# Kernel tuning notes

Hardware: AMD Instinct MI355X
Metric: run time of the kernel (lower is better)

Reference implementation:

```python
import jax, jax.numpy as jnp
import numpy as np

SEQ, HID = 4096, 1024
NEG_INF = -10000000000.0


def setup_inputs() -> dict:
    key = jax.random.key(0)
    ks = jax.random.split(key, 6)
    s = 1.0 / np.sqrt(HID)
    return {
        "query": jax.random.normal(ks[0], (SEQ, HID), jnp.float32),
        "key": jax.random.normal(ks[1], (SEQ, HID), jnp.float32),
        "value": jax.random.normal(ks[2], (SEQ, HID), jnp.float32),
        # SASRec causal mask: allowed positions are 1, masked are 0
        "mask": jnp.tril(jnp.ones((SEQ, SEQ), jnp.int32)),
        "Wq": jax.random.normal(ks[3], (HID, HID), jnp.float32) * s,
        "Wk": jax.random.normal(ks[4], (HID, HID), jnp.float32) * s,
        "Wv": jax.random.normal(ks[5], (HID, HID), jnp.float32) * s,
    }


def reference(query, key, value, mask, Wq, Wk, Wv):
    # nn.Linear(bias=False): y = x @ W.T
    Q = query @ Wq.T   # [S, H]
    K = key @ Wk.T     # [S, H]
    V = value @ Wv.T   # [S, H]
    scale = jnp.sqrt(jnp.asarray(HID, Q.dtype))
    energy = (Q @ K.T) / scale                      # [S, S]
    energy = jnp.where(mask == 0, NEG_INF, energy)  # masked_fill
    attention = jax.nn.softmax(energy, axis=-1)     # [S, S]
    x = attention @ V                               # dropout is identity in eval
    return (x, attention)
```

## Files before the change

kernel.cpp:

```cpp
#include <hip/hip_runtime.h>

#define SEQ 4096
#define HID 1024

typedef _Float16 f16x4 __attribute__((ext_vector_type(4)));
typedef _Float16 f16x8 __attribute__((ext_vector_type(8)));
typedef float    f32x4 __attribute__((ext_vector_type(4)));

__device__ __forceinline__ void gld16(const void* g, void* l) {
    __builtin_amdgcn_global_load_lds(
        (const __attribute__((address_space(1))) unsigned int*)g,
        (__attribute__((address_space(3))) unsigned int*)l, 16, 0, 0);
}

__global__ __launch_bounds__(256) void cast3_f32_f16(
    const float4* __restrict__ a, const float4* __restrict__ b,
    const float4* __restrict__ c,
    f16x4* __restrict__ da, f16x4* __restrict__ db, f16x4* __restrict__ dc,
    int n4) {
    int t = blockIdx.x * 256 + threadIdx.x;
    if (t >= n4) return;
    float4 va = a[t], vb = b[t], vc = c[t];
    f16x4 oa = {(_Float16)va.x, (_Float16)va.y, (_Float16)va.z, (_Float16)va.w};
    f16x4 ob = {(_Float16)vb.x, (_Float16)vb.y, (_Float16)vb.z, (_Float16)vb.w};
    f16x4 oc = {(_Float16)vc.x, (_Float16)vc.y, (_Float16)vc.z, (_Float16)vc.w};
    da[t] = oa; db[t] = ob; dc[t] = oc;
}

__global__ __launch_bounds__(256) void transpose_f16(
    const _Float16* __restrict__ src, _Float16* __restrict__ dst,
    int R, int C) {
    __shared__ _Float16 tile[32][33];
    int c0 = blockIdx.x * 32, r0 = blockIdx.y * 32;
    int tr = threadIdx.x >> 5, tc = threadIdx.x & 31;
#pragma unroll
    for (int q = 0; q < 4; ++q)
        tile[tr + q * 8][tc] = src[(size_t)(r0 + tr + q * 8) * C + c0 + tc];
    __syncthreads();
#pragma unroll
    for (int q = 0; q < 4; ++q)
        dst[(size_t)(c0 + tr + q * 8) * R + r0 + tc] = tile[tc][tr + q * 8];
}

template <typename OutT, bool TRI_SKIP, bool TRI_K, int ZMODE>
__global__ __launch_bounds__(256) void gemm_nt(
    const _Float16* __restrict__ A, const _Float16* __restrict__ Bt,
    OutT* __restrict__ C, int M, int N, int K, float scale,
    long sA, long sB, long sC, int KC) {
    __shared__ __attribute__((aligned(16))) _Float16 As[128 * 32];
    __shared__ __attribute__((aligned(16))) _Float16 Bs[128 * 32];

    const int bm = blockIdx.y, bn = blockIdx.x;
    if (TRI_SKIP && bn > bm) return;
    if (ZMODE == 1) {
        A  += (long)blockIdx.z * sA;
        Bt += (long)blockIdx.z * sB;
        C  += (long)blockIdx.z * sC;
    }
    int kend = TRI_K ? min(K, (bm + 1) * 128) : K;
    int kstart = 0;
    if (ZMODE == 2) {
        kstart = blockIdx.z * KC;
        if (kstart >= kend) return;
        kend = min(kend, kstart + KC);
    }

    const int tid = threadIdx.x;
    const int tr  = tid >> 2;
    const int tc8 = (tid & 3) * 8;

    const _Float16* Ab = A  + (size_t)bm * 128 * K;
    const _Float16* Bb = Bt + (size_t)bn * 128 * K;

    const int wave = tid >> 6;
    const int lane = tid & 63;
    const int wm = (wave >> 1) * 64;
    const int wn = (wave & 1) * 64;
    const int lr = lane & 15;
    const int lk = (lane >> 4) * 8;

    f32x4 acc[4][4];
#pragma unroll
    for (int i = 0; i < 4; ++i)
#pragma unroll
        for (int j = 0; j < 4; ++j) acc[i][j] = (f32x4)0.0f;

    for (int k0 = kstart; k0 < kend; k0 += 32) {
        gld16(Ab + (size_t)tr * K        + k0 + tc8, &As[tr * 32 + tc8]);
        gld16(Ab + (size_t)(64 + tr) * K + k0 + tc8, &As[(64 + tr) * 32 + tc8]);
        gld16(Bb + (size_t)tr * K        + k0 + tc8, &Bs[tr * 32 + tc8]);
        gld16(Bb + (size_t)(64 + tr) * K + k0 + tc8, &Bs[(64 + tr) * 32 + tc8]);
        __syncthreads();

        f16x8 af[4], bfr[4];
#pragma unroll
        for (int i = 0; i < 4; ++i)
            af[i] = *(const f16x8*)&As[(wm + i * 16 + lr) * 32 + lk];
#pragma unroll
        for (int j = 0; j < 4; ++j)
            bfr[j] = *(const f16x8*)&Bs[(wn + j * 16 + lr) * 32 + lk];
#pragma unroll
        for (int i = 0; i < 4; ++i)
#pragma unroll
            for (int j = 0; j < 4; ++j)
                acc[i][j] = __builtin_amdgcn_mfma_f32_16x16x32_f16(
                    af[i], bfr[j], acc[i][j], 0, 0, 0);
        __syncthreads();
    }

    const int er = (lane >> 4) * 4;
    const int ec = lane & 15;
#pragma unroll
    for (int i = 0; i < 4; ++i) {
#pragma unroll
        for (int j = 0; j < 4; ++j) {
            const int row0 = bm * 128 + wm + i * 16 + er;
            const int col  = bn * 128 + wn + j * 16 + ec;
#pragma unroll
            for (int r = 0; r < 4; ++r) {
                const size_t idx = (size_t)(row0 + r) * N + col;
                const float val = acc[i][j][r] * scale;
                if (ZMODE == 2)
                    atomicAdd((float*)&C[idx], val);
                else
                    C[idx] = (OutT)val;
            }
        }
    }
}

__global__ __launch_bounds__(256) void softmax_causal(
    float* __restrict__ E, _Float16* __restrict__ P, int S) {
    __shared__ float rowbuf[SEQ];
    __shared__ float red[8];
    const int i   = blockIdx.x;
    const int tid = threadIdx.x;
    const int wv  = tid >> 6, ln = tid & 63;
    float* Erow = E + (size_t)i * S;

    float lmax = -INFINITY;
    for (int j = tid; j <= i; j += 256) {
        float v = Erow[j];
        rowbuf[j] = v;
        lmax = fmaxf(lmax, v);
    }
#pragma unroll
    for (int o = 32; o > 0; o >>= 1) lmax = fmaxf(lmax, __shfl_down(lmax, o, 64));
    if (ln == 0) red[wv] = lmax;
    __syncthreads();
    if (tid == 0)
        red[4] = fmaxf(fmaxf(red[0], red[1]), fmaxf(red[2], red[3]));
    __syncthreads();
    const float rmax = red[4];

    float lsum = 0.0f;
    for (int j = tid; j <= i; j += 256) {
        float e = __expf(rowbuf[j] - rmax);
        rowbuf[j] = e;
        lsum += e;
    }
#pragma unroll
    for (int o = 32; o > 0; o >>= 1) lsum += __shfl_down(lsum, o, 64);
    __syncthreads();
    if (ln == 0) red[wv] = lsum;
    __syncthreads();
    if (tid == 0)
        red[4] = red[0] + red[1] + red[2] + red[3];
    __syncthreads();
    const float rinv = 1.0f / red[4];

    _Float16* Prow = P + (size_t)i * S;
    for (int j = tid; j < S; j += 256) {
        float a = (j <= i) ? rowbuf[j] * rinv : 0.0f;
        Erow[j] = a;
        Prow[j] = (_Float16)a;
    }
}

extern "C" void kernel_launch(void* const* d_in, const int* in_sizes, int n_in,
                              void* d_out, int out_size, void* d_ws, size_t ws_size,
                              hipStream_t stream) {
    const float* q  = (const float*)d_in[0];
    const float* k  = (const float*)d_in[1];
    const float* v  = (const float*)d_in[2];
    const float* Wq = (const float*)d_in[4];
    const float* Wk = (const float*)d_in[5];
    const float* Wv = (const float*)d_in[6];

    float* out_x   = (float*)d_out;
    float* out_att = out_x + (size_t)SEQ * HID;

    char* ws = (char*)d_ws;
    const size_t SH = (size_t)SEQ * HID * sizeof(_Float16);
    const size_t HH = (size_t)HID * HID * sizeof(_Float16);
    _Float16* qh  = (_Float16*)(ws);
    _Float16* kh  = (_Float16*)(ws + SH);
    _Float16* vh  = (_Float16*)(ws + 2 * SH);
    _Float16* wqh = (_Float16*)(ws + 3 * SH);
    _Float16* wkh = (_Float16*)(ws + 3 * SH + HH);
    _Float16* wvh = (_Float16*)(ws + 3 * SH + 2 * HH);
    _Float16* Qh  = (_Float16*)(ws + 3 * SH + 3 * HH);
    _Float16* Kh  = (_Float16*)(ws + 4 * SH + 3 * HH);
    _Float16* Vh  = (_Float16*)(ws + 5 * SH + 3 * HH);
    _Float16* VT  = (_Float16*)(ws + 6 * SH + 3 * HH);
    _Float16* Ph  = (_Float16*)(ws + 7 * SH + 3 * HH);

    hipMemsetAsync(out_x, 0, (size_t)SEQ * HID * sizeof(float), stream);

    cast3_f32_f16<<<SEQ * HID / 4 / 256, 256, 0, stream>>>(
        (const float4*)q, (const float4*)k, (const float4*)v,
        (f16x4*)qh, (f16x4*)kh, (f16x4*)vh, SEQ * HID / 4);
    cast3_f32_f16<<<HID * HID / 4 / 256, 256, 0, stream>>>(
        (const float4*)Wq, (const float4*)Wk, (const float4*)Wv,
        (f16x4*)wqh, (f16x4*)wkh, (f16x4*)wvh, HID * HID / 4);

    gemm_nt<_Float16, false, false, 1><<<dim3(HID / 128, SEQ / 128, 3), 256, 0, stream>>>(
        qh, wqh, Qh, SEQ, HID, HID, 1.0f,
        (long)SEQ * HID, (long)HID * HID, (long)SEQ * HID, 0);

    transpose_f16<<<dim3(HID / 32, SEQ / 32), 256, 0, stream>>>(Vh, VT, SEQ, HID);

    gemm_nt<float, true, false, 0><<<dim3(SEQ / 128, SEQ / 128), 256, 0, stream>>>(
        Qh, Kh, out_att, SEQ, SEQ, HID, 0.03125f, 0, 0, 0, 0);

    softmax_causal<<<SEQ, 256, 0, stream>>>(out_att, Ph, SEQ);

    gemm_nt<float, false, true, 2><<<dim3(HID / 128, SEQ / 128, 4), 256, 0, stream>>>(
        Ph, VT, out_x, SEQ, HID, SEQ, 1.0f, 0, 0, 0, 1024);
}
```

Before: 331.8 us.

## Store energy in fp16 scratch, merge casts, direct-store single-chunk PV, finer split-K

The QK^T GEMM now writes fp16 energies to a workspace buffer instead of fp32 into the attention output. Softmax reads that buffer, writes fp32 attention once, and overwrites the fp16 buffer in place with probabilities only up to the causal block limit. This drops the fp32 read and the extra write of the full output. The two cast kernels are merged into one launch. The PV split-K is doubled to 8 chunks of 512, and chunks that cover the whole causal range store directly instead of using atomics. Rounding energies to fp16 before softmax adds precision risk, and storing directly on top of the memset is only correct because the output is zeroed first.

```diff
diff --git a/kernel.cpp b/kernel.cpp
--- a/kernel.cpp
+++ b/kernel.cpp
@@ -13,18 +13,27 @@
         (__attribute__((address_space(3))) unsigned int*)l, 16, 0, 0);
 }
 
-__global__ __launch_bounds__(256) void cast3_f32_f16(
-    const float4* __restrict__ a, const float4* __restrict__ b,
-    const float4* __restrict__ c,
-    f16x4* __restrict__ da, f16x4* __restrict__ db, f16x4* __restrict__ dc,
-    int n4) {
+__global__ __launch_bounds__(256) void cast_all(
+    const float4* __restrict__ q, const float4* __restrict__ k,
+    const float4* __restrict__ v,
+    const float4* __restrict__ wq, const float4* __restrict__ wk,
+    const float4* __restrict__ wv,
+    f16x4* __restrict__ qh, f16x4* __restrict__ kh, f16x4* __restrict__ vh,
+    f16x4* __restrict__ wqh, f16x4* __restrict__ wkh, f16x4* __restrict__ wvh,
+    int nX4, int nW4) {
     int t = blockIdx.x * 256 + threadIdx.x;
-    if (t >= n4) return;
-    float4 va = a[t], vb = b[t], vc = c[t];
+    const float4 *a, *b, *c; f16x4 *da, *db, *dc; int idx;
+    if (t < nX4) { a = q; b = k; c = v; da = qh; db = kh; dc = vh; idx = t; }
+    else {
+        idx = t - nX4;
+        if (idx >= nW4) return;
+        a = wq; b = wk; c = wv; da = wqh; db = wkh; dc = wvh;
+    }
+    float4 va = a[idx], vb = b[idx], vc = c[idx];
     f16x4 oa = {(_Float16)va.x, (_Float16)va.y, (_Float16)va.z, (_Float16)va.w};
     f16x4 ob = {(_Float16)vb.x, (_Float16)vb.y, (_Float16)vb.z, (_Float16)vb.w};
     f16x4 oc = {(_Float16)vc.x, (_Float16)vc.y, (_Float16)vc.z, (_Float16)vc.w};
-    da[t] = oa; db[t] = ob; dc[t] = oc;
+    da[idx] = oa; db[idx] = ob; dc[idx] = oc;
 }
 
 __global__ __launch_bounds__(256) void transpose_f16(
@@ -59,9 +68,11 @@
     }
     int kend = TRI_K ? min(K, (bm + 1) * 128) : K;
     int kstart = 0;
+    bool single = false;
     if (ZMODE == 2) {
         kstart = blockIdx.z * KC;
         if (kstart >= kend) return;
+        single = (kend <= KC);
         kend = min(kend, kstart + KC);
     }
 
@@ -120,7 +131,7 @@
             for (int r = 0; r < 4; ++r) {
                 const size_t idx = (size_t)(row0 + r) * N + col;
                 const float val = acc[i][j][r] * scale;
-                if (ZMODE == 2)
+                if (ZMODE == 2 && !single)
                     atomicAdd((float*)&C[idx], val);
                 else
                     C[idx] = (OutT)val;
@@ -130,17 +141,17 @@
 }
 
 __global__ __launch_bounds__(256) void softmax_causal(
-    float* __restrict__ E, _Float16* __restrict__ P, int S) {
+    _Float16* __restrict__ EP, float* __restrict__ att, int S) {
     __shared__ float rowbuf[SEQ];
     __shared__ float red[8];
     const int i   = blockIdx.x;
     const int tid = threadIdx.x;
     const int wv  = tid >> 6, ln = tid & 63;
-    float* Erow = E + (size_t)i * S;
+    _Float16* Erow = EP + (size_t)i * S;
 
     float lmax = -INFINITY;
     for (int j = tid; j <= i; j += 256) {
-        float v = Erow[j];
+        float v = (float)Erow[j];
         rowbuf[j] = v;
         lmax = fmaxf(lmax, v);
     }
@@ -169,11 +180,12 @@
     __syncthreads();
     const float rinv = 1.0f / red[4];
 
-    _Float16* Prow = P + (size_t)i * S;
+    float* arow = att + (size_t)i * S;
+    const int jlim = ((i >> 7) + 1) << 7;
     for (int j = tid; j < S; j += 256) {
         float a = (j <= i) ? rowbuf[j] * rinv : 0.0f;
-        Erow[j] = a;
-        Prow[j] = (_Float16)a;
+        arow[j] = a;
+        if (j < jlim) Erow[j] = (_Float16)a;
     }
 }
 
@@ -203,16 +215,16 @@
     _Float16* Kh  = (_Float16*)(ws + 4 * SH + 3 * HH);
     _Float16* Vh  = (_Float16*)(ws + 5 * SH + 3 * HH);
     _Float16* VT  = (_Float16*)(ws + 6 * SH + 3 * HH);
-    _Float16* Ph  = (_Float16*)(ws + 7 * SH + 3 * HH);
+    _Float16* EP  = (_Float16*)(ws + 7 * SH + 3 * HH);
 
     hipMemsetAsync(out_x, 0, (size_t)SEQ * HID * sizeof(float), stream);
 
-    cast3_f32_f16<<<SEQ * HID / 4 / 256, 256, 0, stream>>>(
+    const int nX4 = SEQ * HID / 4, nW4 = HID * HID / 4;
+    cast_all<<<(nX4 + nW4 + 255) / 256, 256, 0, stream>>>(
         (const float4*)q, (const float4*)k, (const float4*)v,
-        (f16x4*)qh, (f16x4*)kh, (f16x4*)vh, SEQ * HID / 4);
-    cast3_f32_f16<<<HID * HID / 4 / 256, 256, 0, stream>>>(
         (const float4*)Wq, (const float4*)Wk, (const float4*)Wv,
-        (f16x4*)wqh, (f16x4*)wkh, (f16x4*)wvh, HID * HID / 4);
+        (f16x4*)qh, (f16x4*)kh, (f16x4*)vh,
+        (f16x4*)wqh, (f16x4*)wkh, (f16x4*)wvh, nX4, nW4);
 
     gemm_nt<_Float16, false, false, 1><<<dim3(HID / 128, SEQ / 128, 3), 256, 0, stream>>>(
         qh, wqh, Qh, SEQ, HID, HID, 1.0f,
@@ -220,11 +232,11 @@
 
     transpose_f16<<<dim3(HID / 32, SEQ / 32), 256, 0, stream>>>(Vh, VT, SEQ, HID);
 
-    gemm_nt<float, true, false, 0><<<dim3(SEQ / 128, SEQ / 128), 256, 0, stream>>>(
-        Qh, Kh, out_att, SEQ, SEQ, HID, 0.03125f, 0, 0, 0, 0);
-
-    softmax_causal<<<SEQ, 256, 0, stream>>>(out_att, Ph, SEQ);
-
-    gemm_nt<float, false, true, 2><<<dim3(HID / 128, SEQ / 128, 4), 256, 0, stream>>>(
-        Ph, VT, out_x, SEQ, HID, SEQ, 1.0f, 0, 0, 0, 1024);
-}
+    gemm_nt<_Float16, true, false, 0><<<dim3(SEQ / 128, SEQ / 128), 256, 0, stream>>>(
+        Qh, Kh, EP, SEQ, SEQ, HID, 0.03125f, 0, 0, 0, 0);
+
+    softmax_causal<<<SEQ, 256, 0, stream>>>(EP, out_att, SEQ);
+
+    gemm_nt<float, false, true, 2><<<dim3(HID / 128, SEQ / 128, 8), 256, 0, stream>>>(
+        EP, VT, out_x, SEQ, HID, SEQ, 1.0f, 0, 0, 0, 512);
+}
```

After: 354.1 us. 1.07x slower.
